# Optimization experiments

Measured on AMD Instinct MI355X. Metric: run time of the kernel, lower is better.

## Reference

```python
import jax, jax.numpy as jnp
import numpy as np
from functools import partial

KS, SIGMA, K1, K2 = 11, 1.5, 0.01, 0.03
NUM_BLOCKS, BINS = 8, 8


def _gauss_kernel(channels, dtype):
    c = jnp.arange(KS, dtype=dtype) - (KS - 1) / 2.0
    g = jnp.exp(-(c ** 2) / (2.0 * SIGMA ** 2))
    g = g / g.sum()
    k2d = jnp.outer(g, g)  # (KS, KS)
    return jnp.broadcast_to(k2d, (channels, 1, KS, KS))  # OIHW depthwise


def _dwconv(x, k, groups):
    return jax.lax.conv_general_dilated(
        x, k, window_strides=(1, 1), padding='VALID',
        dimension_numbers=('NCHW', 'OIHW', 'NCHW'), feature_group_count=groups)


def _ssim(p, t):
    # torchmetrics default: gaussian 11x11 sigma 1.5, data_range from data, valid region mean
    C = p.shape[1]
    k = _gauss_kernel(C, p.dtype)
    data_range = jnp.maximum(p.max() - p.min(), t.max() - t.min())
    c1 = (K1 * data_range) ** 2
    c2 = (K2 * data_range) ** 2
    mu_p = _dwconv(p, k, C)
    mu_t = _dwconv(t, k, C)
    mu_pp, mu_tt, mu_pt = mu_p * mu_p, mu_t * mu_t, mu_p * mu_t
    sig_p = _dwconv(p * p, k, C) - mu_pp
    sig_t = _dwconv(t * t, k, C) - mu_tt
    sig_pt = _dwconv(p * t, k, C) - mu_pt
    num = (2 * mu_pt + c1) * (2 * sig_pt + c2)
    den = (mu_pp + mu_tt + c1) * (sig_p + sig_t + c2)
    return (num / den).mean()


def _sobel_edges(gray):
    sx = jnp.array([[1, 0, -1], [2, 0, -2], [1, 0, -1]], dtype=gray.dtype).reshape(1, 1, 3, 3)
    sy = jnp.array([[1, 2, 1], [0, 0, 0], [-1, -2, -1]], dtype=gray.dtype).reshape(1, 1, 3, 3)
    k = sx + sy  # conv(x, sx) + conv(x, sy) == conv(x, sx + sy)
    return jax.lax.conv_general_dilated(
        gray, k, window_strides=(1, 1), padding=((1, 1), (1, 1)),
        dimension_numbers=('NCHW', 'OIHW', 'NCHW'))


def _color_histogram(x):
    # torch.histc per channel, bins=8 over [0,1], normalized per channel, concatenated
    B, C, H, W = x.shape
    idx = jnp.clip(jnp.floor(x * BINS).astype(jnp.int32), 0, BINS - 1)
    idx = idx + (jnp.arange(C, dtype=jnp.int32)[None, :, None, None] * BINS)
    counts = jax.ops.segment_sum(jnp.ones_like(x).reshape(-1), idx.reshape(-1),
                                 num_segments=C * BINS)  # (C*BINS,)
    counts = counts.reshape(C, BINS)
    counts = counts / (counts.sum(axis=1, keepdims=True) + 1e-8)
    return counts.reshape(-1)


def _blockwise_mean_color_distance(pred, target):
    B, C, H, W = pred.shape
    bh, bw = H // NUM_BLOCKS, W // NUM_BLOCKS
    pm = pred.reshape(B, C, NUM_BLOCKS, bh, NUM_BLOCKS, bw).mean(axis=(3, 5))   # (B,C,nb,nb)
    tm = target.reshape(B, C, NUM_BLOCKS, bh, NUM_BLOCKS, bw).mean(axis=(3, 5))
    dist = jnp.sqrt(jnp.sum((pm - tm) ** 2, axis=1))  # (B,nb,nb) L2 over channels
    dist_avg = dist.sum(axis=(1, 2)) / (NUM_BLOCKS * NUM_BLOCKS)  # (B,)
    return 1.0 - dist_avg.mean()


def setup_inputs() -> dict:
    key = jax.random.key(0)
    k1, k2 = jax.random.split(key)
    shape = (32, 3, 512, 512)
    pred = jax.random.uniform(k1, shape, dtype=jnp.float32)
    target = jax.random.uniform(k2, shape, dtype=jnp.float32)
    return {"pred": pred, "target": target}


def reference(pred, target):
    ssim = _ssim(pred, target)
    pred_gray = pred.mean(axis=1, keepdims=True)
    target_gray = target.mean(axis=1, keepdims=True)
    edge_ssim = _ssim(_sobel_edges(pred_gray), _sobel_edges(target_gray))
    hist_dist = jnp.sqrt(jnp.sum((_color_histogram(pred) - _color_histogram(target)) ** 2))
    color_reward = 1.0 - hist_dist
    color_distance_reward = _blockwise_mean_color_distance(pred, target)
    reward = (0.25 * ssim + 0.05 * edge_ssim + 0.25 * color_reward
              + 0.45 * color_distance_reward)
    return reward
```

## Files before the change

kernel.cpp:

```cpp
#include <hip/hip_runtime.h>
#include <hip/hip_bf16.h>

#define WS_HIST 0
#define WS_C1   48
#define WS_PART 52
#define WS_DBL  64
#define WS_BSP  72
#define WS_BST  6216
#define WS_MM   12360

#define IMGSZ 262144
#define CH3   786432

__device__ inline float wredS(float v){ for(int o=32;o;o>>=1) v += __shfl_xor(v,o,64); return v; }
__device__ inline float wredMin(float v){ for(int o=32;o;o>>=1) v = fminf(v,__shfl_xor(v,o,64)); return v; }
__device__ inline float wredMax(float v){ for(int o=32;o;o>>=1) v = fmaxf(v,__shfl_xor(v,o,64)); return v; }

__global__ void k_init(unsigned* ws){
    int i = threadIdx.x;
    if (i < 68) ws[i] = 0u;
}

__global__ __launch_bounds__(256) void k_pass1(const float* __restrict__ P,
                                               const float* __restrict__ T,
                                               unsigned* __restrict__ wsU,
                                               float* __restrict__ wsF){
    __shared__ float gP[66][68];
    __shared__ float gT[66][68];
    __shared__ unsigned histSh[4][48];
    __shared__ float bs[6][4];
    __shared__ float ms[8][4];

    const int tid = threadIdx.x, lane = tid & 63, wave = tid >> 6;
    const int bid = blockIdx.x;
    const int b = bid >> 6, sb = bid & 63;
    const int by = sb >> 3, bx = sb & 7;
    const int y0 = by * 64, x0 = bx * 64;
    const int baseB = b * CH3;

    for (int i = tid; i < 4*48; i += 256) ((unsigned*)histSh)[i] = 0u;
    __syncthreads();

    float sp0=0,sp1=0,sp2=0,st0=0,st1=0,st2=0;
    float pmn=1e30f,pmx=-1e30f,tmn=1e30f,tmx=-1e30f;
    for (int k = 0; k < 16; k++){
        int pi = tid + k*256;
        int ly = pi >> 6, lx = pi & 63;
        int off = baseB + (y0+ly)*512 + (x0+lx);
        float p0=P[off], p1=P[off+IMGSZ], p2=P[off+2*IMGSZ];
        float t0=T[off], t1=T[off+IMGSZ], t2=T[off+2*IMGSZ];
        sp0+=p0; sp1+=p1; sp2+=p2; st0+=t0; st1+=t1; st2+=t2;
        pmn = fminf(pmn, fminf(p0, fminf(p1,p2)));
        pmx = fmaxf(pmx, fmaxf(p0, fmaxf(p1,p2)));
        tmn = fminf(tmn, fminf(t0, fminf(t1,t2)));
        tmx = fmaxf(tmx, fmaxf(t0, fmaxf(t1,t2)));
        int b0=(int)floorf(p0*8.f); b0 = b0<0?0:(b0>7?7:b0);
        int b1=(int)floorf(p1*8.f); b1 = b1<0?0:(b1>7?7:b1);
        int b2=(int)floorf(p2*8.f); b2 = b2<0?0:(b2>7?7:b2);
        int c0=(int)floorf(t0*8.f); c0 = c0<0?0:(c0>7?7:c0);
        int c1i=(int)floorf(t1*8.f); c1i = c1i<0?0:(c1i>7?7:c1i);
        int c2i=(int)floorf(t2*8.f); c2i = c2i<0?0:(c2i>7?7:c2i);
        atomicAdd(&histSh[wave][b0], 1u);
        atomicAdd(&histSh[wave][8+b1], 1u);
        atomicAdd(&histSh[wave][16+b2], 1u);
        atomicAdd(&histSh[wave][24+c0], 1u);
        atomicAdd(&histSh[wave][32+c1i], 1u);
        atomicAdd(&histSh[wave][40+c2i], 1u);
        gP[ly+1][lx+1] = (p0+p1+p2)*(1.f/3.f);
        gT[ly+1][lx+1] = (t0+t1+t2)*(1.f/3.f);
    }
    if (tid < 260){
        int ly, lx;
        if (tid < 66){ ly=0; lx=tid; }
        else if (tid < 132){ ly=65; lx=tid-66; }
        else if (tid < 196){ ly=tid-132+1; lx=0; }
        else { ly=tid-196+1; lx=65; }
        int gy = y0-1+ly, gx = x0-1+lx;
        float vp=0.f, vt=0.f;
        if (gy>=0 && gy<512 && gx>=0 && gx<512){
            int off = baseB + gy*512 + gx;
            vp = (P[off]+P[off+IMGSZ]+P[off+2*IMGSZ])*(1.f/3.f);
            vt = (T[off]+T[off+IMGSZ]+T[off+2*IMGSZ])*(1.f/3.f);
        }
        gP[ly][lx]=vp; gT[ly][lx]=vt;
    }
    __syncthreads();

    float emnp=1e30f,emxp=-1e30f,emnt=1e30f,emxt=-1e30f;
    for (int k = 0; k < 16; k++){
        int pi = tid + k*256;
        int ly = (pi>>6)+1, lx = (pi&63)+1;
        float ep = 2.f*(gP[ly-1][lx-1]+gP[ly-1][lx]+gP[ly][lx-1]
                       -gP[ly][lx+1]-gP[ly+1][lx]-gP[ly+1][lx+1]);
        float et = 2.f*(gT[ly-1][lx-1]+gT[ly-1][lx]+gT[ly][lx-1]
                       -gT[ly][lx+1]-gT[ly+1][lx]-gT[ly+1][lx+1]);
        emnp=fminf(emnp,ep); emxp=fmaxf(emxp,ep);
        emnt=fminf(emnt,et); emxt=fmaxf(emxt,et);
    }

    float vals[6] = {sp0,sp1,sp2,st0,st1,st2};
    #pragma unroll
    for (int v=0; v<6; v++){
        float r = wredS(vals[v]);
        if (lane==0) bs[v][wave]=r;
    }
    float mmv[8] = {pmn,pmx,tmn,tmx,emnp,emxp,emnt,emxt};
    #pragma unroll
    for (int v=0; v<8; v++){
        float r = (v&1) ? wredMax(mmv[v]) : wredMin(mmv[v]);
        if (lane==0) ms[v][wave]=r;
    }
    __syncthreads();
    if (tid < 6){
        float s = bs[tid][0]+bs[tid][1]+bs[tid][2]+bs[tid][3];
        int c = tid % 3;
        int o = (tid < 3 ? WS_BSP : WS_BST) + (b*3+c)*64 + sb;
        wsF[o] = s;
    }
    if (tid < 8){
        float a=ms[tid][0], b2=ms[tid][1], c2=ms[tid][2], d2=ms[tid][3];
        float r = (tid&1) ? fmaxf(fmaxf(a,b2),fmaxf(c2,d2))
                          : fminf(fminf(a,b2),fminf(c2,d2));
        wsF[WS_MM + bid*8 + tid] = r;
    }
    if (tid < 48){
        unsigned s = histSh[0][tid]+histSh[1][tid]+histSh[2][tid]+histSh[3][tid];
        atomicAdd(&wsU[WS_HIST + tid], s);
    }
}

__global__ __launch_bounds__(256) void k_fin1(unsigned* __restrict__ wsU,
                                              float* __restrict__ wsF){
    const int tid = threadIdx.x, lane = tid & 63, wave = tid >> 6;
    __shared__ float sh[8][4];
    __shared__ float res[8];
    float mn[4]={1e30f,1e30f,1e30f,1e30f};
    float mx[4]={-1e30f,-1e30f,-1e30f,-1e30f};
    for (int r = tid; r < 2048; r += 256){
        const float* row = &wsF[WS_MM + r*8];
        #pragma unroll
        for (int v=0; v<4; v++){
            mn[v]=fminf(mn[v],row[2*v]); mx[v]=fmaxf(mx[v],row[2*v+1]);
        }
    }
    #pragma unroll
    for (int v=0; v<4; v++){
        float a = wredMin(mn[v]); if (lane==0) sh[2*v][wave]=a;
        float b = wredMax(mx[v]); if (lane==0) sh[2*v+1][wave]=b;
    }
    __syncthreads();
    if (tid < 8){
        float a=sh[tid][0],b=sh[tid][1],c=sh[tid][2],d=sh[tid][3];
        res[tid] = (tid&1) ? fmaxf(fmaxf(a,b),fmaxf(c,d))
                           : fminf(fminf(a,b),fminf(c,d));
    }
    __syncthreads();
    if (tid == 0){
        float dr  = fmaxf(res[1]-res[0], res[3]-res[2]);
        wsF[WS_C1+0] = (0.01f*dr)*(0.01f*dr);
        wsF[WS_C1+1] = (0.03f*dr)*(0.03f*dr);
        float dre = fmaxf(res[5]-res[4], res[7]-res[6]);
        wsF[WS_C1+2] = (0.01f*dre)*(0.01f*dre);
        wsF[WS_C1+3] = (0.03f*dre)*(0.03f*dre);
    }
    float ds = 0.f;
    for (int r = tid; r < 2048; r += 256){
        int b = r >> 6, pos = r & 63;
        float s = 0.f;
        #pragma unroll
        for (int c=0; c<3; c++){
            float pm = wsF[WS_BSP + (b*3+c)*64 + pos] * (1.f/4096.f);
            float tm = wsF[WS_BST + (b*3+c)*64 + pos] * (1.f/4096.f);
            float d = pm - tm; s += d*d;
        }
        ds += sqrtf(s);
    }
    ds = wredS(ds);
    __syncthreads();
    if (lane==0) sh[0][wave] = ds;
    __syncthreads();
    if (tid == 0){
        float total = sh[0][0]+sh[0][1]+sh[0][2]+sh[0][3];
        float cdr = 1.f - total * (1.f/2048.f);
        float d2 = 0.f;
        for (int c=0; c<3; c++){
            float sp=0.f, st=0.f;
            for (int k=0;k<8;k++){ sp += (float)wsU[c*8+k]; st += (float)wsU[24+c*8+k]; }
            for (int k=0;k<8;k++){
                float hp = (float)wsU[c*8+k] / (sp + 1e-8f);
                float ht = (float)wsU[24+c*8+k] / (st + 1e-8f);
                float dd = hp - ht; d2 += dd*dd;
            }
        }
        float creward = 1.f - sqrtf(d2);
        wsF[WS_PART] = 0.25f*creward + 0.45f*cdr;
    }
}

__global__ __launch_bounds__(256) void k_ssim(const float* __restrict__ P,
                                              const float* __restrict__ T,
                                              const float* __restrict__ wsF,
                                              double* __restrict__ ssum){
    __shared__ float sP[42][44];
    __shared__ float sT[42][44];
    __shared__ float hb[5][42][33];
    __shared__ float rr[4];
    const int tid = threadIdx.x;
    const int bid = blockIdx.x;
    const int img = bid >> 8, tile = bid & 255;
    const int ty = tile >> 4, tx = tile & 15;
    const int r0 = ty*32, c0 = tx*32;
    const int base = img * IMGSZ;
    const float c1 = wsF[WS_C1+0], c2 = wsF[WS_C1+1];

    float g[11]; float gs = 0.f;
    #pragma unroll
    for (int i=0;i<11;i++){ float d=(float)(i-5); g[i]=__expf(-d*d*(1.0f/4.5f)); gs+=g[i]; }
    float inv = 1.f/gs;
    #pragma unroll
    for (int i=0;i<11;i++) g[i]*=inv;

    for (int idx = tid; idx < 42*42; idx += 256){
        int ly = idx / 42, lx = idx - ly*42;
        int gy = r0+ly, gx = c0+lx;
        float p=0.f, t=0.f;
        if (gy < 512 && gx < 512){ int o = base + gy*512 + gx; p = P[o]; t = T[o]; }
        sP[ly][lx]=p; sT[ly][lx]=t;
    }
    __syncthreads();
    for (int idx = tid; idx < 42*32; idx += 256){
        int ly = idx >> 5, x = idx & 31;
        float a0=0,a1=0,a2=0,a3=0,a4=0;
        #pragma unroll
        for (int i=0;i<11;i++){
            float p=sP[ly][x+i], t=sT[ly][x+i], w=g[i];
            a0+=w*p; a1+=w*t; a2+=w*p*p; a3+=w*t*t; a4+=w*p*t;
        }
        hb[0][ly][x]=a0; hb[1][ly][x]=a1; hb[2][ly][x]=a2; hb[3][ly][x]=a3; hb[4][ly][x]=a4;
    }
    __syncthreads();
    float acc = 0.f;
    for (int idx = tid; idx < 1024; idx += 256){
        int y = idx >> 5, x = idx & 31;
        float m0=0,m1=0,m2=0,m3=0,m4=0;
        #pragma unroll
        for (int j=0;j<11;j++){
            float w=g[j];
            m0+=w*hb[0][y+j][x]; m1+=w*hb[1][y+j][x]; m2+=w*hb[2][y+j][x];
            m3+=w*hb[3][y+j][x]; m4+=w*hb[4][y+j][x];
        }
        int gy=r0+y, gx=c0+x;
        if (gy < 502 && gx < 502){
            float spv=m2-m0*m0, stv=m3-m1*m1, spt=m4-m0*m1;
            float num=(2.f*m0*m1+c1)*(2.f*spt+c2);
            float den=(m0*m0+m1*m1+c1)*(spv+stv+c2);
            acc += num/den;
        }
    }
    acc = wredS(acc);
    if ((tid&63)==0) rr[tid>>6]=acc;
    __syncthreads();
    if (tid==0) atomicAdd(ssum, (double)(rr[0]+rr[1]+rr[2]+rr[3]));
}

__global__ __launch_bounds__(256) void k_essim(const float* __restrict__ P,
                                               const float* __restrict__ T,
                                               const float* __restrict__ wsF,
                                               double* __restrict__ esum){
    __shared__ float gp[44][46];
    __shared__ float gt[44][46];
    __shared__ float ep[42][44];
    __shared__ float et[42][44];
    __shared__ float hb[5][42][33];
    __shared__ float rr[4];
    const int tid = threadIdx.x;
    const int bid = blockIdx.x;
    const int b = bid >> 8, tile = bid & 255;
    const int ty = tile >> 4, tx = tile & 15;
    const int r0 = ty*32, c0 = tx*32;
    const int base = b * CH3;
    const float c1 = wsF[WS_C1+2], c2 = wsF[WS_C1+3];

    float g[11]; float gs = 0.f;
    #pragma unroll
    for (int i=0;i<11;i++){ float d=(float)(i-5); g[i]=__expf(-d*d*(1.0f/4.5f)); gs+=g[i]; }
    float inv = 1.f/gs;
    #pragma unroll
    for (int i=0;i<11;i++) g[i]*=inv;

    for (int idx = tid; idx < 44*44; idx += 256){
        int ly = idx / 44, lx = idx - ly*44;
        int gy = r0-1+ly, gx = c0-1+lx;
        float vp=0.f, vt=0.f;
        if (gy>=0 && gy<512 && gx>=0 && gx<512){
            int o = base + gy*512 + gx;
            vp = (P[o]+P[o+IMGSZ]+P[o+2*IMGSZ])*(1.f/3.f);
            vt = (T[o]+T[o+IMGSZ]+T[o+2*IMGSZ])*(1.f/3.f);
        }
        gp[ly][lx]=vp; gt[ly][lx]=vt;
    }
    __syncthreads();
    for (int idx = tid; idx < 42*42; idx += 256){
        int ly = idx / 42, lx = idx - ly*42;
        int cy = ly+1, cx = lx+1;
        ep[ly][lx] = 2.f*(gp[cy-1][cx-1]+gp[cy-1][cx]+gp[cy][cx-1]
                         -gp[cy][cx+1]-gp[cy+1][cx]-gp[cy+1][cx+1]);
        et[ly][lx] = 2.f*(gt[cy-1][cx-1]+gt[cy-1][cx]+gt[cy][cx-1]
                         -gt[cy][cx+1]-gt[cy+1][cx]-gt[cy+1][cx+1]);
    }
    __syncthreads();
    for (int idx = tid; idx < 42*32; idx += 256){
        int ly = idx >> 5, x = idx & 31;
        float a0=0,a1=0,a2=0,a3=0,a4=0;
        #pragma unroll
        for (int i=0;i<11;i++){
            float p=ep[ly][x+i], t=et[ly][x+i], w=g[i];
            a0+=w*p; a1+=w*t; a2+=w*p*p; a3+=w*t*t; a4+=w*p*t;
        }
        hb[0][ly][x]=a0; hb[1][ly][x]=a1; hb[2][ly][x]=a2; hb[3][ly][x]=a3; hb[4][ly][x]=a4;
    }
    __syncthreads();
    float acc = 0.f;
    for (int idx = tid; idx < 1024; idx += 256){
        int y = idx >> 5, x = idx & 31;
        float m0=0,m1=0,m2=0,m3=0,m4=0;
        #pragma unroll
        for (int j=0;j<11;j++){
            float w=g[j];
            m0+=w*hb[0][y+j][x]; m1+=w*hb[1][y+j][x]; m2+=w*hb[2][y+j][x];
            m3+=w*hb[3][y+j][x]; m4+=w*hb[4][y+j][x];
        }
        int gy=r0+y, gx=c0+x;
        if (gy < 502 && gx < 502){
            float spv=m2-m0*m0, stv=m3-m1*m1, spt=m4-m0*m1;
            float num=(2.f*m0*m1+c1)*(2.f*spt+c2);
            float den=(m0*m0+m1*m1+c1)*(spv+stv+c2);
            acc += num/den;
        }
    }
    acc = wredS(acc);
    if ((tid&63)==0) rr[tid>>6]=acc;
    __syncthreads();
    if (tid==0) atomicAdd(esum, (double)(rr[0]+rr[1]+rr[2]+rr[3]));
}

__global__ void k_fin2(const float* __restrict__ wsF, unsigned* __restrict__ out){
    const double* d = (const double*)(wsF + WS_DBL);
    double ssim = d[0] / 24192384.0;
    double es   = d[1] / 8064128.0;
    float v = (float)(0.25*ssim + 0.05*es + (double)wsF[WS_PART]);
    unsigned u = __float_as_uint(v);
    unsigned r = (u + 0x7FFFu + ((u>>16)&1u)) >> 16;
    out[0] = r | (r<<16);
}

extern "C" void kernel_launch(void* const* d_in, const int* in_sizes, int n_in,
                              void* d_out, int out_size, void* d_ws, size_t ws_size,
                              hipStream_t stream) {
    const float* P = (const float*)d_in[0];
    const float* T = (const float*)d_in[1];
    float*    wsF = (float*)d_ws;
    unsigned* wsU = (unsigned*)d_ws;
    double*   dbl = (double*)((char*)d_ws + WS_DBL*4);

    k_init  <<<1, 256, 0, stream>>>(wsU);
    k_pass1 <<<2048, 256, 0, stream>>>(P, T, wsU, wsF);
    k_fin1  <<<1, 256, 0, stream>>>(wsU, wsF);
    k_ssim  <<<96*256, 256, 0, stream>>>(P, T, wsF, dbl);
    k_essim <<<32*256, 256, 0, stream>>>(P, T, wsF, dbl+1);
    k_fin2  <<<1, 1, 0, stream>>>(wsF, (unsigned*)d_out);
}
```

Baseline: 750.0 us.

## Register-block separable SSIM passes with float4 LDS loads and transposed intermediates

The horizontal and vertical Gaussian passes of both SSIM kernels are reworked so each thread computes four adjacent outputs from a 16-element register window loaded with float4 LDS reads. Squares and cross products are precomputed once per window, and the intermediate buffer is transposed to [field][x][y] so the vertical pass can also use vector reads. The tile load in k_ssim now uses float4 global loads. This cuts LDS traffic and redundant multiplies, at the cost of higher register pressure and possible LDS bank conflicts on the transposed stores.

Result: no change. 762.5 us (+1.7%).

```diff
diff --git a/kernel.cpp b/kernel.cpp
--- a/kernel.cpp
+++ b/kernel.cpp
@@ -197,15 +197,88 @@
     }
 }
 
+__device__ inline void hpass_4x(const float* sA, const float* sB, const float* g,
+                                float (*hb)[32][44], int njobs , int tid){
+    for (int job = tid; job < njobs; job += 256){
+        int ly = job >> 3, xq = job & 7;
+        const float* ra = sA + ly*44 + xq*4;
+        const float* rb = sB + ly*44 + xq*4;
+        float p[16], t[16];
+        *(float4*)&p[0]  = *(const float4*)&ra[0];
+        *(float4*)&p[4]  = *(const float4*)&ra[4];
+        *(float4*)&p[8]  = *(const float4*)&ra[8];
+        *(float4*)&p[12] = *(const float4*)&ra[12];
+        *(float4*)&t[0]  = *(const float4*)&rb[0];
+        *(float4*)&t[4]  = *(const float4*)&rb[4];
+        *(float4*)&t[8]  = *(const float4*)&rb[8];
+        *(float4*)&t[12] = *(const float4*)&rb[12];
+        float pp[14], tt[14], pt[14];
+        #pragma unroll
+        for (int j=0;j<14;j++){ pp[j]=p[j]*p[j]; tt[j]=t[j]*t[j]; pt[j]=p[j]*t[j]; }
+        float a0[4]={0,0,0,0}, a1[4]={0,0,0,0}, a2[4]={0,0,0,0},
+              a3[4]={0,0,0,0}, a4[4]={0,0,0,0};
+        #pragma unroll
+        for (int i=0;i<11;i++){
+            float w = g[i];
+            #pragma unroll
+            for (int d=0;d<4;d++){
+                a0[d] += w*p[d+i];  a1[d] += w*t[d+i];
+                a2[d] += w*pp[d+i]; a3[d] += w*tt[d+i]; a4[d] += w*pt[d+i];
+            }
+        }
+        #pragma unroll
+        for (int d=0;d<4;d++){
+            int x = xq*4+d;
+            hb[0][x][ly]=a0[d]; hb[1][x][ly]=a1[d]; hb[2][x][ly]=a2[d];
+            hb[3][x][ly]=a3[d]; hb[4][x][ly]=a4[d];
+        }
+    }
+}
+
+__device__ inline float vpass_ssim(const float (*hb)[32][44], const float* g,
+                                   float c1, float c2, int r0, int c0, int tid){
+    int x = tid >> 3, yq = tid & 7;
+    float m[5][4];
+    #pragma unroll
+    for (int f=0; f<5; f++){
+        float v[16];
+        *(float4*)&v[0]  = *(const float4*)&hb[f][x][yq*4];
+        *(float4*)&v[4]  = *(const float4*)&hb[f][x][yq*4+4];
+        *(float4*)&v[8]  = *(const float4*)&hb[f][x][yq*4+8];
+        *(float4*)&v[12] = *(const float4*)&hb[f][x][yq*4+12];
+        #pragma unroll
+        for (int d=0;d<4;d++){
+            float s=0.f;
+            #pragma unroll
+            for (int i=0;i<11;i++) s += g[i]*v[d+i];
+            m[f][d]=s;
+        }
+    }
+    float lsum = 0.f;
+    int gx = c0 + x;
+    #pragma unroll
+    for (int d=0;d<4;d++){
+        int gy = r0 + yq*4 + d;
+        if (gy < 502 && gx < 502){
+            float m0=m[0][d], m1=m[1][d], m2=m[2][d], m3=m[3][d], m4=m[4][d];
+            float spv=m2-m0*m0, stv=m3-m1*m1, spt=m4-m0*m1;
+            float num=(2.f*m0*m1+c1)*(2.f*spt+c2);
+            float den=(m0*m0+m1*m1+c1)*(spv+stv+c2);
+            lsum += num/den;
+        }
+    }
+    return lsum;
+}
+
 __global__ __launch_bounds__(256) void k_ssim(const float* __restrict__ P,
                                               const float* __restrict__ T,
                                               const float* __restrict__ wsF,
                                               double* __restrict__ ssum){
     __shared__ float sP[42][44];
     __shared__ float sT[42][44];
-    __shared__ float hb[5][42][33];
+    __shared__ float hb[5][32][44];
     __shared__ float rr[4];
-    const int tid = threadIdx.x;
+    const int tid = threadIdx.x, lane = tid & 63, wave = tid >> 6;
     const int bid = blockIdx.x;
     const int img = bid >> 8, tile = bid & 255;
     const int ty = tile >> 4, tx = tile & 15;
@@ -220,45 +293,23 @@
     #pragma unroll
     for (int i=0;i<11;i++) g[i]*=inv;
 
-    for (int idx = tid; idx < 42*42; idx += 256){
-        int ly = idx / 42, lx = idx - ly*42;
-        int gy = r0+ly, gx = c0+lx;
-        float p=0.f, t=0.f;
-        if (gy < 512 && gx < 512){ int o = base + gy*512 + gx; p = P[o]; t = T[o]; }
-        sP[ly][lx]=p; sT[ly][lx]=t;
-    }
-    __syncthreads();
-    for (int idx = tid; idx < 42*32; idx += 256){
-        int ly = idx >> 5, x = idx & 31;
-        float a0=0,a1=0,a2=0,a3=0,a4=0;
-        #pragma unroll
-        for (int i=0;i<11;i++){
-            float p=sP[ly][x+i], t=sT[ly][x+i], w=g[i];
-            a0+=w*p; a1+=w*t; a2+=w*p*p; a3+=w*t*t; a4+=w*p*t;
-        }
-        hb[0][ly][x]=a0; hb[1][ly][x]=a1; hb[2][ly][x]=a2; hb[3][ly][x]=a3; hb[4][ly][x]=a4;
-    }
-    __syncthreads();
-    float acc = 0.f;
-    for (int idx = tid; idx < 1024; idx += 256){
-        int y = idx >> 5, x = idx & 31;
-        float m0=0,m1=0,m2=0,m3=0,m4=0;
-        #pragma unroll
-        for (int j=0;j<11;j++){
-            float w=g[j];
-            m0+=w*hb[0][y+j][x]; m1+=w*hb[1][y+j][x]; m2+=w*hb[2][y+j][x];
-            m3+=w*hb[3][y+j][x]; m4+=w*hb[4][y+j][x];
-        }
-        int gy=r0+y, gx=c0+x;
-        if (gy < 502 && gx < 502){
-            float spv=m2-m0*m0, stv=m3-m1*m1, spt=m4-m0*m1;
-            float num=(2.f*m0*m1+c1)*(2.f*spt+c2);
-            float den=(m0*m0+m1*m1+c1)*(spv+stv+c2);
-            acc += num/den;
-        }
-    }
-    acc = wredS(acc);
-    if ((tid&63)==0) rr[tid>>6]=acc;
+    for (int idx = tid; idx < 42*11; idx += 256){
+        int ly = idx / 11, cx = idx - ly*11;
+        int gy = r0+ly, gxb = c0+cx*4;
+        float4 p = {0,0,0,0}, t = {0,0,0,0};
+        if (gy < 512 && gxb < 512){
+            p = *(const float4*)(P + base + gy*512 + gxb);
+            t = *(const float4*)(T + base + gy*512 + gxb);
+        }
+        *(float4*)&sP[ly][cx*4] = p;
+        *(float4*)&sT[ly][cx*4] = t;
+    }
+    __syncthreads();
+    hpass_4x(&sP[0][0], &sT[0][0], g, hb, 336, tid);
+    __syncthreads();
+    float lsum = vpass_ssim(hb, g, c1, c2, r0, c0, tid);
+    lsum = wredS(lsum);
+    if (lane==0) rr[wave]=lsum;
     __syncthreads();
     if (tid==0) atomicAdd(ssum, (double)(rr[0]+rr[1]+rr[2]+rr[3]));
 }
@@ -271,9 +322,9 @@
     __shared__ float gt[44][46];
     __shared__ float ep[42][44];
     __shared__ float et[42][44];
-    __shared__ float hb[5][42][33];
+    __shared__ float hb[5][32][44];
     __shared__ float rr[4];
-    const int tid = threadIdx.x;
+    const int tid = threadIdx.x, lane = tid & 63, wave = tid >> 6;
     const int bid = blockIdx.x;
     const int b = bid >> 8, tile = bid & 255;
     const int ty = tile >> 4, tx = tile & 15;
@@ -309,37 +360,11 @@
                          -gt[cy][cx+1]-gt[cy+1][cx]-gt[cy+1][cx+1]);
     }
     __syncthreads();
-    for (int idx = tid; idx < 42*32; idx += 256){
-        int ly = idx >> 5, x = idx & 31;
-        float a0=0,a1=0,a2=0,a3=0,a4=0;
-        #pragma unroll
-        for (int i=0;i<11;i++){
-            float p=ep[ly][x+i], t=et[ly][x+i], w=g[i];
-            a0+=w*p; a1+=w*t; a2+=w*p*p; a3+=w*t*t; a4+=w*p*t;
-        }
-        hb[0][ly][x]=a0; hb[1][ly][x]=a1; hb[2][ly][x]=a2; hb[3][ly][x]=a3; hb[4][ly][x]=a4;
-    }
-    __syncthreads();
-    float acc = 0.f;
-    for (int idx = tid; idx < 1024; idx += 256){
-        int y = idx >> 5, x = idx & 31;
-        float m0=0,m1=0,m2=0,m3=0,m4=0;
-        #pragma unroll
-        for (int j=0;j<11;j++){
-            float w=g[j];
-            m0+=w*hb[0][y+j][x]; m1+=w*hb[1][y+j][x]; m2+=w*hb[2][y+j][x];
-            m3+=w*hb[3][y+j][x]; m4+=w*hb[4][y+j][x];
-        }
-        int gy=r0+y, gx=c0+x;
-        if (gy < 502 && gx < 502){
-            float spv=m2-m0*m0, stv=m3-m1*m1, spt=m4-m0*m1;
-            float num=(2.f*m0*m1+c1)*(2.f*spt+c2);
-            float den=(m0*m0+m1*m1+c1)*(spv+stv+c2);
-            acc += num/den;
-        }
-    }
-    acc = wredS(acc);
-    if ((tid&63)==0) rr[tid>>6]=acc;
+    hpass_4x(&ep[0][0], &et[0][0], g, hb, 336, tid);
+    __syncthreads();
+    float lsum = vpass_ssim(hb, g, c1, c2, r0, c0, tid);
+    lsum = wredS(lsum);
+    if (lane==0) rr[wave]=lsum;
     __syncthreads();
     if (tid==0) atomicAdd(esum, (double)(rr[0]+rr[1]+rr[2]+rr[3]));
 }
```
